# Performance work log

Hardware: AMD Instinct MI355X
Metric: run time of the kernel (lower is better)

The kernel has to match this reference:

```python
import jax, jax.numpy as jnp
import numpy as np

N_LEVELS = 7
N_HEADS = 2
HIDDEN = 128
LP_P = 4.0  # LPPool1d norm


def setup_inputs() -> dict:
    key = jax.random.key(0)
    ks = jax.random.split(key, 9)
    B, S, H = 2048, 200, HIDDEN
    item_seq = jax.random.randint(ks[0], (B, S), 0, 100)
    item_seq_emb = jax.random.normal(ks[1], (B, S, H), dtype=jnp.float32)
    item_seq_len = jax.random.randint(ks[2], (B,), 0, S)
    scale = 0.02
    W_lq = jax.random.normal(ks[3], (H, H), dtype=jnp.float32) * scale
    b_lq = jnp.zeros((H,), dtype=jnp.float32)
    Wq = jax.random.normal(ks[4], (H, H), dtype=jnp.float32) * scale
    bq = jnp.zeros((H,), dtype=jnp.float32)
    Wk = jax.random.normal(ks[5], (H, H), dtype=jnp.float32) * scale
    bk = jnp.zeros((H,), dtype=jnp.float32)
    return {"item_seq": item_seq, "item_seq_emb": item_seq_emb,
            "item_seq_len": item_seq_len, "W_lq": W_lq, "b_lq": b_lq,
            "Wq": Wq, "bq": bq, "Wk": Wk, "bk": bk}


def reference(item_seq, item_seq_emb, item_seq_len, W_lq, b_lq, Wq, bq, Wk, bk):
    B, S, H = item_seq_emb.shape
    nh, L = N_HEADS, N_LEVELS
    d = H // nh
    mask = item_seq > 0  # [B,S]

    # multi-level gather of last j+1 positions; torch clamp(-1) + index -1 == last pos
    j = jnp.arange(L)
    idx = jnp.clip(item_seq_len[:, None] - (j[None, :] + 1), -1, 1000)  # [B,L]
    idx = jnp.where(idx < 0, idx + S, idx)
    gathered = jnp.take_along_axis(item_seq_emb, idx[:, :, None], axis=1)  # [B,L,H]
    level_emb = jnp.cumsum(gathered, axis=1)  # level i = sum of gathers 0..i

    # shared level-query linear (ModuleList([lin]*L) aliases one Linear)
    queries = level_emb @ W_lq.T + b_lq  # [B,L,H]

    # raw torch .view() reshapes replicated exactly
    q = (queries @ Wq.T + bq).reshape(B * nh, L, d)
    k = (item_seq_emb @ Wk.T + bk).reshape(B * nh, S, d)
    v = item_seq_emb.reshape(B, S, nh, d)

    alpha = jax.nn.sigmoid(jnp.einsum('bld,bsd->bls', q, k))  # [B*nh, L, S]
    alpha = alpha.reshape(B, nh * L, S).transpose(0, 2, 1)  # [B, S, nh*L]
    alpha = jax.nn.softmax(alpha, axis=1)

    # LPPool1d(p=4, kernel=L, stride=L) over last dim -> [B,S,nh]
    alpha = alpha.reshape(B, S, nh, L)
    alpha = jnp.sum(alpha ** LP_P, axis=-1) ** (1.0 / LP_P)

    alpha = jnp.where(mask[:, :, None], alpha, -jnp.inf)
    alpha = jax.nn.softmax(alpha, axis=1)  # dropout off (inference)

    weighted = (alpha[..., None] * v).reshape(B, S, H) * mask[:, :, None].astype(item_seq_emb.dtype)
    return jnp.sum(weighted, axis=1)  # [B,H]
```

## Files before the change

### kernel.cpp

```cpp
#include <hip/hip_runtime.h>
#include <hip/hip_bf16.h>

#define SEQ 200
#define HID 128
#define NLVL 7

#define WS_M16_W 0
#define WS_BF    32768
#define WS_VB    33280
#define WS_CB    33792
#define WS_WC    33796
#define WS_BC    50180
#define WS_WORDS 50308

#define SCST 212

typedef __attribute__((ext_vector_type(8))) short short8;
typedef __attribute__((ext_vector_type(4))) float f32x4;

__device__ __forceinline__ float bf_lo(unsigned u) { return __uint_as_float(u << 16); }
__device__ __forceinline__ float bf_hi(unsigned u) { return __uint_as_float(u & 0xffff0000u); }
__device__ __forceinline__ unsigned short bf_bits(float f) {
    __hip_bfloat16 h = __float2bfloat16(f);
    return *reinterpret_cast<unsigned short*>(&h);
}
__device__ __forceinline__ unsigned pack_bf(float a, float b) {
    return (unsigned)bf_bits(a) | ((unsigned)bf_bits(b) << 16);
}
__device__ __forceinline__ short8 cvt8(float4 a, float4 b) {
    short8 f;
    f[0] = (short)bf_bits(a.x); f[1] = (short)bf_bits(a.y);
    f[2] = (short)bf_bits(a.z); f[3] = (short)bf_bits(a.w);
    f[4] = (short)bf_bits(b.x); f[5] = (short)bf_bits(b.y);
    f[6] = (short)bf_bits(b.z); f[7] = (short)bf_bits(b.w);
    return f;
}

__global__ __launch_bounds__(256) void precomp0(
    const float* __restrict__ Wlq, const float* __restrict__ blq,
    const float* __restrict__ Wq,  const float* __restrict__ bq,
    float* __restrict__ ws)
{
    int id = blockIdx.x * 256 + threadIdx.x;
    int r = id >> 7, j = id & 127;
    float acc = 0.f;
    #pragma unroll 8
    for (int c = 0; c < 128; ++c) acc += Wq[r * 128 + c] * Wlq[c * 128 + j];
    ws[WS_WC + id] = acc;
    if (id < 128) {
        float b = bq[id];
        #pragma unroll 8
        for (int c = 0; c < 128; ++c) b += Wq[id * 128 + c] * blq[c];
        ws[WS_BC + id] = b;
    }
}

__global__ __launch_bounds__(256) void precomp1(
    const float* __restrict__ Wk, const float* __restrict__ bk, float* __restrict__ ws)
{
    int gid = blockIdx.x * 256 + threadIdx.x;
    if (gid < 65536) {
        int j = gid & 127, c = (gid >> 7) & 127, g = gid >> 14;
        int u = g >> 1, par = g & 1;
        const float* wc = ws + WS_WC + u * 64 * 128 + j;
        const float* wk = Wk + par * 64 * 128 + c;
        float acc = 0.f;
        #pragma unroll 8
        for (int d = 0; d < 64; ++d) acc += wc[d * 128] * wk[d * 128];
        ((__hip_bfloat16*)ws)[gid] = __float2bfloat16(acc);
    } else if (gid < 66048) {
        int t = gid - 65536, c = t & 127, g = t >> 7;
        int u = g >> 1, par = g & 1;
        float acc = 0.f;
        #pragma unroll 8
        for (int d = 0; d < 64; ++d)
            acc += ws[WS_BC + u * 64 + d] * Wk[(par * 64 + d) * 128 + c];
        ws[WS_BF + t] = acc;
    } else if (gid < 66560) {
        int t = gid - 66048, j = t & 127, g = t >> 7;
        int u = g >> 1, par = g & 1;
        float acc = 0.f;
        #pragma unroll 8
        for (int d = 0; d < 64; ++d)
            acc += ws[WS_WC + (u * 64 + d) * 128 + j] * bk[par * 64 + d];
        ws[WS_VB + t] = acc;
    } else if (gid < 66564) {
        int g = gid - 66560, u = g >> 1, par = g & 1;
        float acc = 0.f;
        for (int d = 0; d < 64; ++d)
            acc += ws[WS_BC + u * 64 + d] * bk[par * 64 + d];
        ws[WS_CB + g] = acc;
    }
}

__global__ __launch_bounds__(512, 8) void mixer_main(
    const int* __restrict__ item_seq,
    const float* __restrict__ emb,
    const int* __restrict__ seq_len,
    const float* __restrict__ ws,
    float* __restrict__ out)
{
    const int b    = blockIdx.x;
    const int tid  = threadIdx.x;
    const int wave = tid >> 6, lane = tid & 63;
    const int ln   = lane & 15, quad = lane >> 4;

    __shared__ __align__(16) short s_qkhi[30 * 136];
    __shared__ __align__(16) short s_qklo[30 * 136];
    __shared__ __align__(16) char  s_region[14 * SCST * 4];
    __shared__ float s_qb[28];
    __shared__ float s_denom[14];
    __shared__ __align__(16) float s_A[2 * SEQ];
    __shared__ __align__(16) float s_red[512];

    float* s_scores = (float*)s_region;
    float* s_lvl    = (float*)s_region;
    short* s_lvl16  = (short*)(s_region + 3584);

    const float* embb = emb + (size_t)b * SEQ * HID;
    const int len = seq_len[b];

    if (tid < HID) {
        float e[NLVL];
        #pragma unroll
        for (int j = 0; j < NLVL; ++j) {
            int idx = len - (j + 1);
            if (idx < 0) idx = SEQ - 1;
            e[j] = embb[(size_t)idx * HID + tid];
        }
        float acc = 0.f;
        #pragma unroll
        for (int j = 0; j < NLVL; ++j) {
            acc += e[j];
            s_lvl[j * HID + tid] = acc;
            s_lvl16[j * 136 + tid] = (short)bf_bits(acc);
        }
    } else if (tid < 196) {
        int t = tid - 128;
        ((uint2*)(s_qkhi + 28 * 136))[t] = make_uint2(0u, 0u);
        ((uint2*)(s_qklo + 28 * 136))[t] = make_uint2(0u, 0u);
    } else if (tid < 210) {
        s_denom[tid - 196] = 0.f;
    }
    __syncthreads();

    {
        const int g = wave >> 1, halfm = wave & 1;
        const int mrow = ln;
        short8 bfrag[4];
        #pragma unroll
        for (int k = 0; k < 4; ++k)
            bfrag[k] = *(const short8*)(s_lvl16 + mrow * 136 + k * 32 + quad * 8);
        const short* M16 = (const short*)ws;
        #pragma unroll
        for (int mt = 0; mt < 4; ++mt) {
            int mtile = halfm * 4 + mt;
            int cbase = mtile * 16 + quad * 4;
            f32x4 acc;
            #pragma unroll
            for (int r = 0; r < 4; ++r) acc[r] = ws[WS_BF + g * 128 + cbase + r];
            const short* Ab = M16 + (g * 128 + mtile * 16 + mrow) * 128;
            #pragma unroll
            for (int k = 0; k < 4; ++k) {
                short8 afrag = *(const short8*)(Ab + k * 32 + quad * 8);
                acc = __builtin_amdgcn_mfma_f32_16x16x32_bf16(afrag, bfrag[k], acc, 0, 0, 0);
            }
            if (mrow < NLVL) {
                int qrow = mrow * 4 + g;
                unsigned h01 = pack_bf(acc[0], acc[1]);
                unsigned h23 = pack_bf(acc[2], acc[3]);
                float l0 = acc[0] - bf_lo(h01), l1 = acc[1] - bf_hi(h01);
                float l2 = acc[2] - bf_lo(h23), l3 = acc[3] - bf_hi(h23);
                *(uint2*)(s_qkhi + qrow * 136 + cbase) = make_uint2(h01, h23);
                *(uint2*)(s_qklo + qrow * 136 + cbase) = make_uint2(pack_bf(l0, l1), pack_bf(l2, l3));
            }
        }
        if (tid < 448) {
            int grp = tid >> 4, sub = tid & 15;
            int gg = grp & 3, L = grp >> 2;
            const float* vb = ws + WS_VB + gg * 128;
            const float* lv = s_lvl + L * 128;
            float acc = 0.f;
            #pragma unroll
            for (int k = 0; k < 8; ++k) {
                int j = sub + 16 * k;
                acc += lv[j] * vb[j];
            }
            acc += __shfl_xor(acc, 1, 16);
            acc += __shfl_xor(acc, 2, 16);
            acc += __shfl_xor(acc, 4, 16);
            acc += __shfl_xor(acc, 8, 16);
            if (sub == 0) s_qb[grp] = acc + ws[WS_CB + gg];
        }
    }
    __syncthreads();

    {
        #pragma unroll 1
        for (int t = wave; t < 14; t += 8) {
            const int h = t / 7, mtile = t % 7;
            int gqrow = mtile * 16 + ln;
            int rowg = h * 100 + (gqrow < 100 ? gqrow : 99);
            const float* Arow = embb + (size_t)rowg * HID;
            float qbv = (ln < 14) ? s_qb[h * 14 + ln] : 0.f;
            f32x4 acc;
            acc[0] = qbv; acc[1] = qbv; acc[2] = qbv; acc[3] = qbv;
            #pragma unroll 2
            for (int kk = 0; kk < 4; ++kk) {
                float4 v0 = *(const float4*)(Arow + kk * 32 + quad * 8);
                float4 v1 = *(const float4*)(Arow + kk * 32 + quad * 8 + 4);
                short8 afrag = cvt8(v0, v1);
                const int boff = (h * 14 + ln) * 136 + kk * 32 + quad * 8;
                short8 bhi = *(const short8*)(s_qkhi + boff);
                short8 blo = *(const short8*)(s_qklo + boff);
                acc = __builtin_amdgcn_mfma_f32_16x16x32_bf16(afrag, bhi, acc, 0, 0, 0);
                acc = __builtin_amdgcn_mfma_f32_16x16x32_bf16(afrag, blo, acc, 0, 0, 0);
            }
            float part = 0.f;
            if (ln < 14) {
                int srow = (h * 7 + (ln >> 1)) * SCST, par = ln & 1;
                #pragma unroll
                for (int i = 0; i < 4; ++i) {
                    int gq = mtile * 16 + quad * 4 + i;
                    if (gq < 100) {
                        float sg = 1.f / (1.f + __expf(-acc[i]));
                        float E = __expf(sg);
                        s_scores[srow + 2 * gq + par] = E;
                        part += E;
                    }
                }
            }
            part += __shfl_xor(part, 16, 64);
            part += __shfl_xor(part, 32, 64);
            part += __shfl_xor(part, 1, 64);
            if (quad == 0 && ln < 14 && (ln & 1) == 0)
                atomicAdd(&s_denom[h * 7 + (ln >> 1)], part);
        }
    }
    __syncthreads();

    if (tid < 2 * SEQ) {
        int h = tid / SEQ, s2 = tid % SEQ;
        float ssum = 0.f;
        #pragma unroll
        for (int l = 0; l < NLVL; ++l) {
            float v = __fdividef(s_scores[(h * NLVL + l) * SCST + s2],
                                 s_denom[h * NLVL + l]);
            float v2 = v * v;
            ssum += v2 * v2;
        }
        float A = sqrtf(sqrtf(ssum));
        int m = item_seq[(size_t)b * SEQ + s2];
        s_A[tid] = (m > 0) ? __expf(A) : 0.f;
    }
    __syncthreads();

    {
        int c = tid & 127, qq = tid >> 7;
        int h = c >> 6;
        const float* wv = s_A + h * SEQ + qq * 50;
        const float* eg = embb + (size_t)(qq * 50) * HID + c;
        float acc = 0.f;
        #pragma unroll 10
        for (int s = 0; s < 50; ++s)
            acc += wv[s] * eg[(size_t)s * HID];
        s_red[tid] = acc;
    }
    __syncthreads();

    if (tid < HID) {
        int h = tid >> 6;
        const float* row = s_A + h * SEQ;
        float sum = row[lane] + row[lane + 64] + row[lane + 128]
                  + ((lane + 192 < 200) ? row[lane + 192] : 0.f);
        #pragma unroll
        for (int mm = 1; mm < 64; mm <<= 1) sum += __shfl_xor(sum, mm, 64);
        float inv = 1.f / sum;
        float tot = (s_red[tid] + s_red[tid + 128] + s_red[tid + 256] + s_red[tid + 384]) * inv;
        out[(size_t)b * HID + tid] = tot;
    }
}

__global__ __launch_bounds__(256) void mixer_fallback(
    const int* __restrict__ item_seq, const float* __restrict__ emb,
    const int* __restrict__ seq_len,
    const float* __restrict__ Wlq, const float* __restrict__ blq,
    const float* __restrict__ Wq,  const float* __restrict__ bq,
    const float* __restrict__ Wk,  const float* __restrict__ bk,
    float* __restrict__ out)
{
    const int b = blockIdx.x, tid = threadIdx.x;
    __shared__ unsigned s_embu[SEQ * 65];
    __shared__ float s_qk[28 * 128];
    __shared__ float s_qb[28];
    __shared__ float s_tmp[2800];
    __shared__ float s_A[400];
    __shared__ float s_red[256];
    __shared__ float s_inv[2];

    {
        const float4* src = (const float4*)(emb + (size_t)b * SEQ * HID);
        for (int i = tid; i < SEQ * 32; i += 256) {
            int row = i >> 5, j = i & 31;
            float4 v = src[i];
            unsigned* dst = s_embu + row * 65 + 2 * j;
            dst[0] = pack_bf(v.x, v.y);
            dst[1] = pack_bf(v.z, v.w);
        }
    }
    const int len = seq_len[b];
    if (tid < HID) {
        float acc = 0.f;
        for (int j = 0; j < NLVL; ++j) {
            int idx = len - (j + 1);
            if (idx < 0) idx = SEQ - 1;
            acc += emb[(size_t)b * SEQ * HID + (size_t)idx * HID + tid];
            s_tmp[j * HID + tid] = acc;
        }
    }
    __syncthreads();
    for (int t = tid; t < NLVL * HID; t += 256) {
        int l = t >> 7, c = t & 127;
        const float* x = s_tmp + l * HID;
        float acc = blq[c];
        #pragma unroll 8
        for (int k = 0; k < HID; ++k) acc += x[k] * Wlq[c * HID + k];
        s_tmp[896 + t] = acc;
    }
    __syncthreads();
    for (int t = tid; t < NLVL * HID; t += 256) {
        int l = t >> 7, c = t & 127;
        const float* x = s_tmp + 896 + l * HID;
        float acc = bq[c];
        #pragma unroll 8
        for (int k = 0; k < HID; ++k) acc += x[k] * Wq[c * HID + k];
        s_tmp[t] = acc;
    }
    __syncthreads();
    for (int o = tid; o < 28 * 128; o += 256) {
        int qrow = o >> 7, c = o & 127;
        int hl = qrow >> 1, par = qrow & 1;
        const float* qv = s_tmp + hl * 64;
        float acc = 0.f;
        #pragma unroll 8
        for (int d2 = 0; d2 < 64; ++d2) acc += qv[d2] * Wk[(par * 64 + d2) * HID + c];
        s_qk[qrow * 128 + c] = acc;
    }
    if (tid < 28) {
        int hl = tid >> 1, par = tid & 1;
        float acc = 0.f;
        for (int d2 = 0; d2 < 64; ++d2) acc += s_tmp[hl * 64 + d2] * bk[par * 64 + d2];
        s_qb[tid] = acc;
    }
    __syncthreads();
    for (int o = tid; o < 700; o += 256) {
        int hl = o / 50, g = o % 50;
        int h = (hl >= 7) ? 1 : 0;
        int rA = h * 100 + g, rB = rA + 50;
        const unsigned* eA = s_embu + rA * 65;
        const unsigned* eB = s_embu + rB * 65;
        const float* k0 = s_qk + (hl * 2) * 128;
        const float* k1 = s_qk + (hl * 2 + 1) * 128;
        float a0 = 0.f, a1 = 0.f, c0a = 0.f, c1a = 0.f;
        #pragma unroll 4
        for (int kk = 0; kk < 64; ++kk) {
            unsigned uA = eA[kk], uB = eB[kk];
            float2 w0 = *(const float2*)(k0 + 2 * kk);
            float2 w1 = *(const float2*)(k1 + 2 * kk);
            float alo = bf_lo(uA), ahi = bf_hi(uA);
            float blo = bf_lo(uB), bhi = bf_hi(uB);
            a0 += alo * w0.x + ahi * w0.y;  a1 += alo * w1.x + ahi * w1.y;
            c0a += blo * w0.x + bhi * w0.y; c1a += blo * w1.x + bhi * w1.y;
        }
        float qb0 = s_qb[hl * 2], qb1 = s_qb[hl * 2 + 1];
        float* row = s_tmp + hl * 200;
        row[2 * g]       = 1.f / (1.f + __expf(-(a0 + qb0)));
        row[2 * g + 1]   = 1.f / (1.f + __expf(-(a1 + qb1)));
        row[2 * g + 100] = 1.f / (1.f + __expf(-(c0a + qb0)));
        row[2 * g + 101] = 1.f / (1.f + __expf(-(c1a + qb1)));
    }
    __syncthreads();
    const int wave = tid >> 6, lane = tid & 63;
    for (int r = wave; r < 14; r += 4) {
        float* row = s_tmp + r * 200;
        float e0 = __expf(row[lane]), e1 = __expf(row[lane + 64]);
        float e2 = __expf(row[lane + 128]);
        float e3 = (lane + 192 < 200) ? __expf(row[lane + 192]) : 0.f;
        float sum = e0 + e1 + e2 + e3;
        #pragma unroll
        for (int m = 1; m < 64; m <<= 1) sum += __shfl_xor(sum, m, 64);
        float inv = 1.f / sum;
        row[lane] = e0 * inv; row[lane + 64] = e1 * inv; row[lane + 128] = e2 * inv;
        if (lane + 192 < 200) row[lane + 192] = e3 * inv;
    }
    __syncthreads();
    for (int o = tid; o < 2 * SEQ; o += 256) {
        int h = o / SEQ, s2 = o % SEQ;
        float ssum = 0.f;
        #pragma unroll
        for (int l = 0; l < NLVL; ++l) {
            float v = s_tmp[(h * NLVL + l) * 200 + s2];
            float v2 = v * v; ssum += v2 * v2;
        }
        float A = sqrtf(sqrtf(ssum));
        s_A[o] = (item_seq[(size_t)b * SEQ + s2] > 0) ? __expf(A) : 0.f;
    }
    __syncthreads();
    if (wave < 2) {
        const float* row = s_A + wave * SEQ;
        float sum = row[lane] + row[lane + 64] + row[lane + 128]
                  + ((lane + 192 < 200) ? row[lane + 192] : 0.f);
        #pragma unroll
        for (int m = 1; m < 64; m <<= 1) sum += __shfl_xor(sum, m, 64);
        if (lane == 0) s_inv[wave] = 1.f / sum;
    }
    __syncthreads();
    {
        int c = tid & 127, halfb = tid >> 7;
        int h = c >> 6;
        const float* wv = s_A + h * SEQ + halfb * 100;
        float acc = 0.f;
        #pragma unroll 4
        for (int s2 = 0; s2 < 100; ++s2) {
            unsigned u = s_embu[(halfb * 100 + s2) * 65 + (c >> 1)];
            acc += wv[s2] * ((c & 1) ? bf_hi(u) : bf_lo(u));
        }
        s_red[tid] = acc;
    }
    __syncthreads();
    if (tid < HID) {
        int h = tid >> 6;
        out[(size_t)b * HID + tid] = (s_red[tid] + s_red[tid + 128]) * s_inv[h];
    }
}

extern "C" void kernel_launch(void* const* d_in, const int* in_sizes, int n_in,
                              void* d_out, int out_size, void* d_ws, size_t ws_size,
                              hipStream_t stream) {
    const int* item_seq = (const int*)d_in[0];
    const float* emb    = (const float*)d_in[1];
    const int* seq_len  = (const int*)d_in[2];
    const float* Wlq    = (const float*)d_in[3];
    const float* blq    = (const float*)d_in[4];
    const float* Wq     = (const float*)d_in[5];
    const float* bq     = (const float*)d_in[6];
    const float* Wk     = (const float*)d_in[7];
    const float* bk     = (const float*)d_in[8];
    float* out          = (float*)d_out;
    const int B = in_sizes[2];

    if (ws_size >= (size_t)WS_WORDS * 4) {
        float* ws = (float*)d_ws;
        precomp0<<<64, 256, 0, stream>>>(Wlq, blq, Wq, bq, ws);
        precomp1<<<261, 256, 0, stream>>>(Wk, bk, ws);
        mixer_main<<<B, 512, 0, stream>>>(item_seq, emb, seq_len, ws, out);
    } else {
        mixer_fallback<<<B, 256, 0, stream>>>(item_seq, emb, seq_len, Wlq, blq, Wq, bq, Wk, bk, out);
    }
}
```

Before: 344.5 us.

## Split mixer_main per head: launch two blocks per batch row

The main kernel now launches 2*B blocks, with each block handling one of the two heads for a batch row. Shared-memory buffers shrink to a single head's worth, the score stage uses 7 waves with no loop, and the final weighted sum covers 64 columns split into 8 sequence chunks. This doubles the parallelism and reduces LDS per block, which may raise occupancy. The cost is that both blocks redo the level gather and the level-query MFMA for every row (each block discards half of the result), and each row's item_seq and embedding data is read twice.

```diff
diff --git a/kernel.cpp b/kernel.cpp
--- a/kernel.cpp
+++ b/kernel.cpp
@@ -100,17 +100,18 @@
     const float* __restrict__ ws,
     float* __restrict__ out)
 {
-    const int b    = blockIdx.x;
+    const int bid  = blockIdx.x;
+    const int b    = bid >> 1, h = bid & 1;
     const int tid  = threadIdx.x;
     const int wave = tid >> 6, lane = tid & 63;
     const int ln   = lane & 15, quad = lane >> 4;
 
-    __shared__ __align__(16) short s_qkhi[30 * 136];
-    __shared__ __align__(16) short s_qklo[30 * 136];
-    __shared__ __align__(16) char  s_region[14 * SCST * 4];
-    __shared__ float s_qb[28];
-    __shared__ float s_denom[14];
-    __shared__ __align__(16) float s_A[2 * SEQ];
+    __shared__ __align__(16) short s_qkhi[16 * 136];
+    __shared__ __align__(16) short s_qklo[16 * 136];
+    __shared__ __align__(16) char  s_region[7936];
+    __shared__ float s_qb[14];
+    __shared__ float s_denom[7];
+    __shared__ __align__(16) float s_A[SEQ];
     __shared__ __align__(16) float s_red[512];
 
     float* s_scores = (float*)s_region;
@@ -137,9 +138,9 @@
         }
     } else if (tid < 196) {
         int t = tid - 128;
-        ((uint2*)(s_qkhi + 28 * 136))[t] = make_uint2(0u, 0u);
-        ((uint2*)(s_qklo + 28 * 136))[t] = make_uint2(0u, 0u);
-    } else if (tid < 210) {
+        ((uint2*)(s_qkhi + 14 * 136))[t] = make_uint2(0u, 0u);
+        ((uint2*)(s_qklo + 14 * 136))[t] = make_uint2(0u, 0u);
+    } else if (tid < 203) {
         s_denom[tid - 196] = 0.f;
     }
     __syncthreads();
@@ -165,19 +166,21 @@
                 short8 afrag = *(const short8*)(Ab + k * 32 + quad * 8);
                 acc = __builtin_amdgcn_mfma_f32_16x16x32_bf16(afrag, bfrag[k], acc, 0, 0, 0);
             }
-            if (mrow < NLVL) {
-                int qrow = mrow * 4 + g;
+            int qrow = mrow * 4 + g;
+            int ql = qrow - h * 14;
+            if (mrow < NLVL && ql >= 0 && ql < 14) {
                 unsigned h01 = pack_bf(acc[0], acc[1]);
                 unsigned h23 = pack_bf(acc[2], acc[3]);
                 float l0 = acc[0] - bf_lo(h01), l1 = acc[1] - bf_hi(h01);
                 float l2 = acc[2] - bf_lo(h23), l3 = acc[3] - bf_hi(h23);
-                *(uint2*)(s_qkhi + qrow * 136 + cbase) = make_uint2(h01, h23);
-                *(uint2*)(s_qklo + qrow * 136 + cbase) = make_uint2(pack_bf(l0, l1), pack_bf(l2, l3));
+                *(uint2*)(s_qkhi + ql * 136 + cbase) = make_uint2(h01, h23);
+                *(uint2*)(s_qklo + ql * 136 + cbase) = make_uint2(pack_bf(l0, l1), pack_bf(l2, l3));
             }
         }
-        if (tid < 448) {
+        if (tid < 224) {
             int grp = tid >> 4, sub = tid & 15;
-            int gg = grp & 3, L = grp >> 2;
+            int qrow = h * 14 + grp;
+            int gg = qrow & 3, L = qrow >> 2;
             const float* vb = ws + WS_VB + gg * 128;
             const float* lv = s_lvl + L * 128;
             float acc = 0.f;
@@ -195,89 +198,84 @@
     }
     __syncthreads();
 
-    {
-        #pragma unroll 1
-        for (int t = wave; t < 14; t += 8) {
-            const int h = t / 7, mtile = t % 7;
-            int gqrow = mtile * 16 + ln;
-            int rowg = h * 100 + (gqrow < 100 ? gqrow : 99);
-            const float* Arow = embb + (size_t)rowg * HID;
-            float qbv = (ln < 14) ? s_qb[h * 14 + ln] : 0.f;
-            f32x4 acc;
-            acc[0] = qbv; acc[1] = qbv; acc[2] = qbv; acc[3] = qbv;
-            #pragma unroll 2
-            for (int kk = 0; kk < 4; ++kk) {
-                float4 v0 = *(const float4*)(Arow + kk * 32 + quad * 8);
-                float4 v1 = *(const float4*)(Arow + kk * 32 + quad * 8 + 4);
-                short8 afrag = cvt8(v0, v1);
-                const int boff = (h * 14 + ln) * 136 + kk * 32 + quad * 8;
-                short8 bhi = *(const short8*)(s_qkhi + boff);
-                short8 blo = *(const short8*)(s_qklo + boff);
-                acc = __builtin_amdgcn_mfma_f32_16x16x32_bf16(afrag, bhi, acc, 0, 0, 0);
-                acc = __builtin_amdgcn_mfma_f32_16x16x32_bf16(afrag, blo, acc, 0, 0, 0);
-            }
-            float part = 0.f;
-            if (ln < 14) {
-                int srow = (h * 7 + (ln >> 1)) * SCST, par = ln & 1;
-                #pragma unroll
-                for (int i = 0; i < 4; ++i) {
-                    int gq = mtile * 16 + quad * 4 + i;
-                    if (gq < 100) {
-                        float sg = 1.f / (1.f + __expf(-acc[i]));
-                        float E = __expf(sg);
-                        s_scores[srow + 2 * gq + par] = E;
-                        part += E;
-                    }
+    if (wave < 7) {
+        const int mtile = wave;
+        int gqrow = mtile * 16 + ln;
+        int rowg = h * 100 + (gqrow < 100 ? gqrow : 99);
+        const float* Arow = embb + (size_t)rowg * HID;
+        float qbv = (ln < 14) ? s_qb[ln] : 0.f;
+        f32x4 acc;
+        acc[0] = qbv; acc[1] = qbv; acc[2] = qbv; acc[3] = qbv;
+        #pragma unroll 2
+        for (int kk = 0; kk < 4; ++kk) {
+            float4 v0 = *(const float4*)(Arow + kk * 32 + quad * 8);
+            float4 v1 = *(const float4*)(Arow + kk * 32 + quad * 8 + 4);
+            short8 afrag = cvt8(v0, v1);
+            const int boff = ln * 136 + kk * 32 + quad * 8;
+            short8 bhi = *(const short8*)(s_qkhi + boff);
+            short8 blo = *(const short8*)(s_qklo + boff);
+            acc = __builtin_amdgcn_mfma_f32_16x16x32_bf16(afrag, bhi, acc, 0, 0, 0);
+            acc = __builtin_amdgcn_mfma_f32_16x16x32_bf16(afrag, blo, acc, 0, 0, 0);
+        }
+        float part = 0.f;
+        if (ln < 14) {
+            int srow = (ln >> 1) * SCST, par = ln & 1;
+            #pragma unroll
+            for (int i = 0; i < 4; ++i) {
+                int gq = mtile * 16 + quad * 4 + i;
+                if (gq < 100) {
+                    float sg = 1.f / (1.f + __expf(-acc[i]));
+                    float E = __expf(sg);
+                    s_scores[srow + 2 * gq + par] = E;
+                    part += E;
                 }
             }
-            part += __shfl_xor(part, 16, 64);
-            part += __shfl_xor(part, 32, 64);
-            part += __shfl_xor(part, 1, 64);
-            if (quad == 0 && ln < 14 && (ln & 1) == 0)
-                atomicAdd(&s_denom[h * 7 + (ln >> 1)], part);
-        }
-    }
-    __syncthreads();
-
-    if (tid < 2 * SEQ) {
-        int h = tid / SEQ, s2 = tid % SEQ;
+        }
+        part += __shfl_xor(part, 16, 64);
+        part += __shfl_xor(part, 32, 64);
+        part += __shfl_xor(part, 1, 64);
+        if (quad == 0 && ln < 14 && (ln & 1) == 0)
+            atomicAdd(&s_denom[ln >> 1], part);
+    }
+    __syncthreads();
+
+    if (tid < SEQ) {
+        int s2 = tid;
         float ssum = 0.f;
         #pragma unroll
         for (int l = 0; l < NLVL; ++l) {
-            float v = __fdividef(s_scores[(h * NLVL + l) * SCST + s2],
-                                 s_denom[h * NLVL + l]);
+            float v = __fdividef(s_scores[l * SCST + s2], s_denom[l]);
             float v2 = v * v;
             ssum += v2 * v2;
         }
         float A = sqrtf(sqrtf(ssum));
         int m = item_seq[(size_t)b * SEQ + s2];
-        s_A[tid] = (m > 0) ? __expf(A) : 0.f;
+        s_A[s2] = (m > 0) ? __expf(A) : 0.f;
     }
     __syncthreads();
 
     {
-        int c = tid & 127, qq = tid >> 7;
-        int h = c >> 6;
-        const float* wv = s_A + h * SEQ + qq * 50;
-        const float* eg = embb + (size_t)(qq * 50) * HID + c;
-        float acc = 0.f;
-        #pragma unroll 10
-        for (int s = 0; s < 50; ++s)
+        int c64 = tid & 63, qq = tid >> 6;
+        const float* wv = s_A + qq * 25;
+        const float* eg = embb + (size_t)(qq * 25) * HID + h * 64 + c64;
+        float acc = 0.f;
+        #pragma unroll 5
+        for (int s = 0; s < 25; ++s)
             acc += wv[s] * eg[(size_t)s * HID];
-        s_red[tid] = acc;
-    }
-    __syncthreads();
-
-    if (tid < HID) {
-        int h = tid >> 6;
-        const float* row = s_A + h * SEQ;
-        float sum = row[lane] + row[lane + 64] + row[lane + 128]
-                  + ((lane + 192 < 200) ? row[lane + 192] : 0.f);
-        #pragma unroll
-        for (int mm = 1; mm < 64; mm <<= 1) sum += __shfl_xor(sum, mm, 64);
-        float inv = 1.f / sum;
-        float tot = (s_red[tid] + s_red[tid + 128] + s_red[tid + 256] + s_red[tid + 384]) * inv;
-        out[(size_t)b * HID + tid] = tot;
+        s_red[qq * 64 + c64] = acc;
+    }
+    __syncthreads();
+
+    if (tid < 64) {
+        float a = s_A[tid] + s_A[tid + 64] + s_A[tid + 128]
+                + ((tid < 8) ? s_A[tid + 192] : 0.f);
+        #pragma unroll
+        for (int mm = 1; mm < 64; mm <<= 1) a += __shfl_xor(a, mm, 64);
+        float inv = 1.f / a;
+        float red = 0.f;
+        #pragma unroll
+        for (int q = 0; q < 8; ++q) red += s_red[q * 64 + tid];
+        out[(size_t)b * HID + h * 64 + tid] = red * inv;
     }
 }
 
@@ -453,7 +451,7 @@
         float* ws = (float*)d_ws;
         precomp0<<<64, 256, 0, stream>>>(Wlq, blq, Wq, bq, ws);
         precomp1<<<261, 256, 0, stream>>>(Wk, bk, ws);
-        mixer_main<<<B, 512, 0, stream>>>(item_seq, emb, seq_len, ws, out);
+        mixer_main<<<2 * B, 512, 0, stream>>>(item_seq, emb, seq_len, ws, out);
     } else {
         mixer_fallback<<<B, 256, 0, stream>>>(item_seq, emb, seq_len, Wlq, blq, Wq, bq, Wk, bk, out);
     }
```

New measurement: 360.2 us. +4.6%, slower.
